# Optimization experiments

Hardware: AMD Instinct MI355X
Metric: run time of the kernel (lower is better)

## Reference

```python
import jax, jax.numpy as jnp
import numpy as np

NUM_NODES = 100000
E = 512    # embedding_size
U = 64     # embedding_u_size
T = 8      # edge_type_count
A = 32     # dim_a
B = 8192   # batch
NB = 10    # neighbors per type


def setup_inputs() -> dict:
    key = jax.random.key(0)
    ks = jax.random.split(key, 8)
    std = 1.0 / np.sqrt(E)
    return {
        "node_embeddings": jax.random.uniform(ks[0], (NUM_NODES, E), jnp.float32, -1.0, 1.0),
        "node_type_embeddings": jax.random.uniform(ks[1], (NUM_NODES, T, U), jnp.float32, -1.0, 1.0),
        "trans_weights": jax.random.normal(ks[2], (T, U, E), jnp.float32) * std,
        "trans_weights_s1": jax.random.normal(ks[3], (T, U, A), jnp.float32) * std,
        "trans_weights_s2": jax.random.normal(ks[4], (T, A, 1), jnp.float32) * std,
        "train_inputs": jax.random.randint(ks[5], (B,), 0, NUM_NODES, jnp.int32),
        "train_types": jax.random.randint(ks[6], (B,), 0, T, jnp.int32),
        "node_neigh": jax.random.randint(ks[7], (B, T, NB), 0, NUM_NODES, jnp.int32),
    }


def reference(node_embeddings, node_type_embeddings, trans_weights,
              trans_weights_s1, trans_weights_s2,
              train_inputs, train_types, node_neigh):
    # node_embed: [B, E]
    node_embed = node_embeddings[train_inputs]
    # Per-type neighbor gather. Original materializes [B,T,NB,T,U] then takes the
    # diagonal over the two type axes; we gather only the diagonal directly:
    # neigh_embed[b,t,n,:] = node_type_embeddings[node_neigh[b,t,n], t, :]
    type_idx = jnp.arange(T)[None, :, None]              # [1,T,1]
    neigh_embed = node_type_embeddings[node_neigh, type_idx]  # [B,T,NB,U]
    node_type_embed = neigh_embed.sum(axis=2)            # [B,T,U]

    # Per-sample gathered projection weights (MoE-style by edge type)
    w_s1 = trans_weights_s1[train_types]                 # [B,U,A]
    w_s2 = trans_weights_s2[train_types]                 # [B,A,1]
    w = trans_weights[train_types]                       # [B,U,E]

    # attention over edge types
    h = jnp.tanh(jnp.einsum('btu,bua->bta', node_type_embed, w_s1))  # [B,T,A]
    scores = jnp.einsum('bta,bao->bt', h, w_s2)          # [B,T] (squeeze of [B,T,1])
    attention = jax.nn.softmax(scores, axis=-1)          # [B,T]

    agg = jnp.einsum('bt,btu->bu', attention, node_type_embed)  # [B,U]
    node_embed = node_embed + jnp.einsum('bu,bue->be', agg, w)  # [B,E]

    # F.normalize(dim=1): divide by L2 norm clamped at 1e-12
    norm = jnp.maximum(jnp.linalg.norm(node_embed, axis=1, keepdims=True), 1e-12)
    return node_embed / norm
```

## Files before the change

### kernel.cpp

```cpp
#include <hip/hip_runtime.h>

#define E_DIM 512
#define U_DIM 64
#define T_DIM 8
#define A_DIM 32
#define NB    10
#define BATCH 8192

__launch_bounds__(256, 8)
__global__ void gatne_kernel(
    const float* __restrict__ node_embeddings,
    const float* __restrict__ node_type_embeddings,
    const float* __restrict__ trans_weights,
    const float* __restrict__ trans_weights_s1,
    const float* __restrict__ trans_weights_s2,
    const int*   __restrict__ train_inputs,
    const int*   __restrict__ train_types,
    const int*   __restrict__ node_neigh,
    float*       __restrict__ out)
{
    const int b    = blockIdx.x;
    const int tid  = threadIdx.x;
    const int lane = tid & 63;
    const int wv   = tid >> 6;

    __shared__ float s_nte[T_DIM][U_DIM];
    __shared__ float s_att[T_DIM];
    __shared__ float s_agg[U_DIM];
    __shared__ float s_red[4];

    const int* nn = node_neigh + (size_t)b * (T_DIM * NB);
    int my = 0;
    if (lane < 2 * NB) my = nn[wv * NB + (lane < NB ? lane : 30 + lane)];

    const int ni = train_inputs[b];
    const int ty = train_types[b];

    const int e0 = tid * 2;
    const float2 ne = *(const float2*)(node_embeddings + (size_t)ni * E_DIM + e0);

    float a0 = 0.f, a1 = 0.f;
    #pragma unroll
    for (int n = 0; n < NB; ++n) {
        const int i0 = __shfl(my, n, 64);
        const int i1 = __shfl(my, NB + n, 64);
        a0 += node_type_embeddings[(size_t)i0 * (T_DIM * U_DIM) + wv * U_DIM + lane];
        a1 += node_type_embeddings[(size_t)i1 * (T_DIM * U_DIM) + (wv + 4) * U_DIM + lane];
    }
    s_nte[wv][lane]     = a0;
    s_nte[wv + 4][lane] = a1;
    __syncthreads();

    {
        const int t = tid >> 5;
        const int a = tid & 31;
        const float* w1 = trans_weights_s1 + (size_t)ty * (U_DIM * A_DIM) + a;
        float h = 0.f;
        #pragma unroll
        for (int u = 0; u < U_DIM; ++u)
            h = fmaf(s_nte[t][u], w1[u * A_DIM], h);
        float val = tanhf(h) * trans_weights_s2[ty * A_DIM + a];
        #pragma unroll
        for (int off = 16; off > 0; off >>= 1)
            val += __shfl_down(val, off, 32);
        if (a == 0) s_att[t] = val;
    }
    __syncthreads();

    if (tid < U_DIM) {
        float sc0 = s_att[0], sc1 = s_att[1], sc2 = s_att[2], sc3 = s_att[3];
        float sc4 = s_att[4], sc5 = s_att[5], sc6 = s_att[6], sc7 = s_att[7];
        const float m = fmaxf(fmaxf(fmaxf(sc0, sc1), fmaxf(sc2, sc3)),
                              fmaxf(fmaxf(sc4, sc5), fmaxf(sc6, sc7)));
        const float x0 = __expf(sc0 - m), x1 = __expf(sc1 - m);
        const float x2 = __expf(sc2 - m), x3 = __expf(sc3 - m);
        const float x4 = __expf(sc4 - m), x5 = __expf(sc5 - m);
        const float x6 = __expf(sc6 - m), x7 = __expf(sc7 - m);
        const float inv_sum = 1.f / (x0 + x1 + x2 + x3 + x4 + x5 + x6 + x7);
        const float acc = x0 * s_nte[0][tid] + x1 * s_nte[1][tid]
                        + x2 * s_nte[2][tid] + x3 * s_nte[3][tid]
                        + x4 * s_nte[4][tid] + x5 * s_nte[5][tid]
                        + x6 * s_nte[6][tid] + x7 * s_nte[7][tid];
        s_agg[tid] = acc * inv_sum;
    }
    __syncthreads();

    const float* wb = trans_weights + (size_t)ty * (U_DIM * E_DIM) + e0;
    float v0 = ne.x, v1 = ne.y;
    #pragma unroll 16
    for (int u = 0; u < U_DIM; ++u) {
        const float av = s_agg[u];
        const float2 w2v = *(const float2*)(wb + (size_t)u * E_DIM);
        v0 = fmaf(av, w2v.x, v0);
        v1 = fmaf(av, w2v.y, v1);
    }

    float ss = v0 * v0 + v1 * v1;
    #pragma unroll
    for (int off = 32; off > 0; off >>= 1)
        ss += __shfl_xor(ss, off, 64);
    if (lane == 0) s_red[wv] = ss;
    __syncthreads();
    const float total = s_red[0] + s_red[1] + s_red[2] + s_red[3];
    const float inv = 1.f / fmaxf(sqrtf(total), 1e-12f);

    float2 o; o.x = v0 * inv; o.y = v1 * inv;
    *(float2*)(out + (size_t)b * E_DIM + e0) = o;
}

extern "C" void kernel_launch(void* const* d_in, const int* in_sizes, int n_in,
                              void* d_out, int out_size, void* d_ws, size_t ws_size,
                              hipStream_t stream) {
    const float* node_embeddings      = (const float*)d_in[0];
    const float* node_type_embeddings = (const float*)d_in[1];
    const float* trans_weights        = (const float*)d_in[2];
    const float* trans_weights_s1     = (const float*)d_in[3];
    const float* trans_weights_s2     = (const float*)d_in[4];
    const int*   train_inputs         = (const int*)d_in[5];
    const int*   train_types          = (const int*)d_in[6];
    const int*   node_neigh           = (const int*)d_in[7];
    float* out = (float*)d_out;

    gatne_kernel<<<BATCH, 256, 0, stream>>>(
        node_embeddings, node_type_embeddings, trans_weights,
        trans_weights_s1, trans_weights_s2,
        train_inputs, train_types, node_neigh, out);
}
```

Measured before the change: 416.7 us.

## Bucket samples by edge type and process four same-type samples per block

```diff
diff --git a/kernel.cpp b/kernel.cpp
--- a/kernel.cpp
+++ b/kernel.cpp
@@ -6,9 +6,226 @@
 #define A_DIM 32
 #define NB    10
 #define BATCH 8192
+#define G     4
+#define MAX_BLOCKS (BATCH / G + T_DIM)
+
+#define WS_PERM  0
+#define WS_START 8192
+#define WS_BLK   8201
+#define WS_INTS  8210
+
+__global__ void bucket_kernel(const int* __restrict__ train_types,
+                              int* __restrict__ ws)
+{
+    __shared__ int cnt[T_DIM], offs[T_DIM], startS[T_DIM];
+    const int tid  = threadIdx.x;
+    const int lane = tid & 63;
+
+    if (tid < T_DIM) { cnt[tid] = 0; offs[tid] = 0; }
+    __syncthreads();
+
+    int ty[8];
+    #pragma unroll
+    for (int it = 0; it < 8; ++it) ty[it] = train_types[tid + it * 1024];
+
+    #pragma unroll
+    for (int it = 0; it < 8; ++it) {
+        #pragma unroll
+        for (int t = 0; t < T_DIM; ++t) {
+            const unsigned long long m = __ballot(ty[it] == t);
+            if (m && lane == __ffsll((unsigned long long)m) - 1)
+                atomicAdd(&cnt[t], __popcll(m));
+        }
+    }
+    __syncthreads();
+
+    if (tid == 0) {
+        int s = 0, bs = 0;
+        for (int t = 0; t < T_DIM; ++t) {
+            startS[t] = s;
+            ws[WS_START + t] = s;
+            ws[WS_BLK + t]   = bs;
+            s  += cnt[t];
+            bs += (cnt[t] + G - 1) / G;
+        }
+        ws[WS_START + T_DIM] = s;
+        ws[WS_BLK + T_DIM]   = bs;
+    }
+    __syncthreads();
+
+    #pragma unroll
+    for (int it = 0; it < 8; ++it) {
+        const int idx = tid + it * 1024;
+        const int t   = ty[it];
+        #pragma unroll
+        for (int tt = 0; tt < T_DIM; ++tt) {
+            const unsigned long long m = __ballot(t == tt);
+            if (t == tt) {
+                const int leader = __ffsll((unsigned long long)m) - 1;
+                int base;
+                if (lane == leader) base = atomicAdd(&offs[tt], __popcll(m));
+                base = __shfl(base, leader, 64);
+                const int rank = __popcll(m & ((1ull << lane) - 1ull));
+                ws[WS_PERM + startS[tt] + base + rank] = idx;
+            }
+        }
+    }
+}
 
 __launch_bounds__(256, 8)
-__global__ void gatne_kernel(
+__global__ void gatne_main(
+    const float* __restrict__ node_embeddings,
+    const float* __restrict__ node_type_embeddings,
+    const float* __restrict__ trans_weights,
+    const float* __restrict__ trans_weights_s1,
+    const float* __restrict__ trans_weights_s2,
+    const int*   __restrict__ train_inputs,
+    const int*   __restrict__ node_neigh,
+    const int*   __restrict__ ws,
+    float*       __restrict__ out)
+{
+    const int tid  = threadIdx.x;
+    const int lane = tid & 63;
+    const int wv   = tid >> 6;
+
+    __shared__ float s_nte[G][T_DIM][U_DIM];
+    __shared__ __align__(16) float s_agg[U_DIM][G];
+    __shared__ float s_red[4][G];
+
+    const int j = blockIdx.x;
+    if (j >= ws[WS_BLK + T_DIM]) return;
+
+    int t = 0;
+    #pragma unroll
+    for (int k = 1; k < T_DIM; ++k) if (j >= ws[WS_BLK + k]) t = k;
+    const int eStart = ws[WS_START + t];
+    const int eEnd   = ws[WS_START + t + 1];
+    const int eBase  = eStart + (j - ws[WS_BLK + t]) * G;
+    const int nE     = min(G, eEnd - eBase);
+
+    int eIdx[G];
+    #pragma unroll
+    for (int g = 0; g < G; ++g)
+        eIdx[g] = ws[WS_PERM + eBase + min(g, nE - 1)];
+
+    const int e0 = tid * 2;
+    float2 ne[G];
+    #pragma unroll
+    for (int g = 0; g < G; ++g)
+        ne[g] = *(const float2*)(node_embeddings + (size_t)train_inputs[eIdx[g]] * E_DIM + e0);
+
+    const int myE = (wv == 0) ? eIdx[0] : (wv == 1) ? eIdx[1] : (wv == 2) ? eIdx[2] : eIdx[3];
+
+    const int* nn = node_neigh + (size_t)myE * (T_DIM * NB);
+    const int i0 = nn[lane];
+    const int i1 = (lane < (T_DIM * NB - 64)) ? nn[64 + lane] : 0;
+    float acc[T_DIM];
+    #pragma unroll
+    for (int tt = 0; tt < T_DIM; ++tt) {
+        float a = 0.f;
+        #pragma unroll
+        for (int n = 0; n < NB; ++n) {
+            const int jj  = tt * NB + n;
+            const int nbi = (jj < 64) ? __shfl(i0, jj, 64) : __shfl(i1, jj - 64, 64);
+            a += node_type_embeddings[(size_t)nbi * (T_DIM * U_DIM) + tt * U_DIM + lane];
+        }
+        acc[tt] = a;
+        s_nte[wv][tt][lane] = a;
+    }
+    __builtin_amdgcn_wave_barrier();
+
+    const int a_idx = lane & 31;
+    const int half  = lane >> 5;
+    const float* w1 = trans_weights_s1 + (size_t)t * (U_DIM * A_DIM) + a_idx;
+    float h0 = 0.f, h1 = 0.f, h2 = 0.f, h3 = 0.f;
+    #pragma unroll
+    for (int u = 0; u < U_DIM; ++u) {
+        const float wv1 = w1[u * A_DIM];
+        h0 = fmaf(s_nte[wv][half + 0][u], wv1, h0);
+        h1 = fmaf(s_nte[wv][half + 2][u], wv1, h1);
+        h2 = fmaf(s_nte[wv][half + 4][u], wv1, h2);
+        h3 = fmaf(s_nte[wv][half + 6][u], wv1, h3);
+    }
+    const float w2v = trans_weights_s2[t * A_DIM + a_idx];
+    h0 = tanhf(h0) * w2v;  h1 = tanhf(h1) * w2v;
+    h2 = tanhf(h2) * w2v;  h3 = tanhf(h3) * w2v;
+    #pragma unroll
+    for (int off = 16; off > 0; off >>= 1) {
+        h0 += __shfl_down(h0, off, 32);
+        h1 += __shfl_down(h1, off, 32);
+        h2 += __shfl_down(h2, off, 32);
+        h3 += __shfl_down(h3, off, 32);
+    }
+    const float sc0 = __shfl(h0, 0, 64),  sc2 = __shfl(h1, 0, 64);
+    const float sc4 = __shfl(h2, 0, 64),  sc6 = __shfl(h3, 0, 64);
+    const float sc1 = __shfl(h0, 32, 64), sc3 = __shfl(h1, 32, 64);
+    const float sc5 = __shfl(h2, 32, 64), sc7 = __shfl(h3, 32, 64);
+
+    const float m = fmaxf(fmaxf(fmaxf(sc0, sc1), fmaxf(sc2, sc3)),
+                          fmaxf(fmaxf(sc4, sc5), fmaxf(sc6, sc7)));
+    const float x0 = __expf(sc0 - m), x1 = __expf(sc1 - m);
+    const float x2 = __expf(sc2 - m), x3 = __expf(sc3 - m);
+    const float x4 = __expf(sc4 - m), x5 = __expf(sc5 - m);
+    const float x6 = __expf(sc6 - m), x7 = __expf(sc7 - m);
+    const float inv_sum = 1.f / (x0 + x1 + x2 + x3 + x4 + x5 + x6 + x7);
+
+    const float agg = (x0 * acc[0] + x1 * acc[1] + x2 * acc[2] + x3 * acc[3] +
+                       x4 * acc[4] + x5 * acc[5] + x6 * acc[6] + x7 * acc[7]) * inv_sum;
+    s_agg[lane][wv] = agg;
+    __syncthreads();
+
+    const float* wb = trans_weights + (size_t)t * (U_DIM * E_DIM) + e0;
+    float2 v0 = ne[0], v1 = ne[1], v2 = ne[2], v3 = ne[3];
+    #pragma unroll 16
+    for (int u = 0; u < U_DIM; ++u) {
+        const float2 wv2 = *(const float2*)(wb + (size_t)u * E_DIM);
+        const float4 ag  = *(const float4*)(&s_agg[u][0]);
+        v0.x = fmaf(ag.x, wv2.x, v0.x);  v0.y = fmaf(ag.x, wv2.y, v0.y);
+        v1.x = fmaf(ag.y, wv2.x, v1.x);  v1.y = fmaf(ag.y, wv2.y, v1.y);
+        v2.x = fmaf(ag.z, wv2.x, v2.x);  v2.y = fmaf(ag.z, wv2.y, v2.y);
+        v3.x = fmaf(ag.w, wv2.x, v3.x);  v3.y = fmaf(ag.w, wv2.y, v3.y);
+    }
+
+    float ss0 = v0.x * v0.x + v0.y * v0.y;
+    float ss1 = v1.x * v1.x + v1.y * v1.y;
+    float ss2 = v2.x * v2.x + v2.y * v2.y;
+    float ss3 = v3.x * v3.x + v3.y * v3.y;
+    #pragma unroll
+    for (int off = 32; off > 0; off >>= 1) {
+        ss0 += __shfl_xor(ss0, off, 64);
+        ss1 += __shfl_xor(ss1, off, 64);
+        ss2 += __shfl_xor(ss2, off, 64);
+        ss3 += __shfl_xor(ss3, off, 64);
+    }
+    if (lane == 0) {
+        s_red[wv][0] = ss0; s_red[wv][1] = ss1;
+        s_red[wv][2] = ss2; s_red[wv][3] = ss3;
+    }
+    __syncthreads();
+    float tot[G];
+    #pragma unroll
+    for (int g = 0; g < G; ++g)
+        tot[g] = s_red[0][g] + s_red[1][g] + s_red[2][g] + s_red[3][g];
+
+    const float iv0 = 1.f / fmaxf(sqrtf(tot[0]), 1e-12f);
+    const float iv1 = 1.f / fmaxf(sqrtf(tot[1]), 1e-12f);
+    const float iv2 = 1.f / fmaxf(sqrtf(tot[2]), 1e-12f);
+    const float iv3 = 1.f / fmaxf(sqrtf(tot[3]), 1e-12f);
+
+    {
+        float2 o; o.x = v0.x * iv0; o.y = v0.y * iv0;
+        *(float2*)(out + (size_t)eIdx[0] * E_DIM + e0) = o;
+    }
+    if (1 < nE) { float2 o; o.x = v1.x * iv1; o.y = v1.y * iv1;
+                  *(float2*)(out + (size_t)eIdx[1] * E_DIM + e0) = o; }
+    if (2 < nE) { float2 o; o.x = v2.x * iv2; o.y = v2.y * iv2;
+                  *(float2*)(out + (size_t)eIdx[2] * E_DIM + e0) = o; }
+    if (3 < nE) { float2 o; o.x = v3.x * iv3; o.y = v3.y * iv3;
+                  *(float2*)(out + (size_t)eIdx[3] * E_DIM + e0) = o; }
+}
+
+__launch_bounds__(256, 8)
+__global__ void gatne_fallback(
     const float* __restrict__ node_embeddings,
     const float* __restrict__ node_type_embeddings,
     const float* __restrict__ trans_weights,
@@ -35,7 +252,6 @@
 
     const int ni = train_inputs[b];
     const int ty = train_types[b];
-
     const int e0 = tid * 2;
     const float2 ne = *(const float2*)(node_embeddings + (size_t)ni * E_DIM + e0);
 
@@ -121,8 +337,16 @@
     const int*   node_neigh           = (const int*)d_in[7];
     float* out = (float*)d_out;
 
-    gatne_kernel<<<BATCH, 256, 0, stream>>>(
-        node_embeddings, node_type_embeddings, trans_weights,
-        trans_weights_s1, trans_weights_s2,
-        train_inputs, train_types, node_neigh, out);
+    if (d_ws != nullptr && ws_size >= WS_INTS * sizeof(int)) {
+        bucket_kernel<<<1, 1024, 0, stream>>>(train_types, (int*)d_ws);
+        gatne_main<<<MAX_BLOCKS, 256, 0, stream>>>(
+            node_embeddings, node_type_embeddings, trans_weights,
+            trans_weights_s1, trans_weights_s2,
+            train_inputs, node_neigh, (const int*)d_ws, out);
+    } else {
+        gatne_fallback<<<BATCH, 256, 0, stream>>>(
+            node_embeddings, node_type_embeddings, trans_weights,
+            trans_weights_s1, trans_weights_s2,
+            train_inputs, train_types, node_neigh, out);
+    }
 }
```

Result: slower. 681.1 us (+63.5%).
